# Kernel optimization log

Hardware: AMD Instinct MI355X
Metric: run time of the kernel (lower is better)

The kernel has to match this reference:

```python
import jax, jax.numpy as jnp
import numpy as np

B, NP, L, C, NA = 16, 512, 20, 3, 50
RATIO = 0.8
K = int(np.ceil(RATIO * NP))  # 410 nodes kept per graph
N = B * NP
E = 6 * N
NF, EF = 13, 4
EPS = 1e-5


def _graph_norm(x, w, b, ms):
    # PyG GraphNorm called WITHOUT batch in the source -> single global graph
    mean = x.mean(0)
    out = x - ms * mean
    var = (out * out).mean(0)
    return w * out / jnp.sqrt(var + EPS) + b


def _forward(x, pan_w, lin1_w, lin1_b, norm1_w, norm1_b, norm1_ms,
             pool_p, pool_beta, gat_wl, gat_bl, gat_wr, gat_br, gat_att, gat_bias,
             norm2_w, norm2_b, norm2_ms,
             val1_w, val1_b, val2_w, val2_b, val3_w, val3_b,
             adv1_w, adv1_b, adv2_w, adv2_b, adv3_w, adv3_b,
             edge_index, current_node_ids, action_mask):
    src, dst = edge_index[0], edge_index[1]
    # PANConv builds SparseTensor(row=edge_index[1], col=edge_index[0]) -> row = target
    A = jnp.zeros((B, NP, NP), x.dtype).at[dst // NP, dst % NP, src % NP].set(1.0)
    eyeB = jnp.broadcast_to(jnp.eye(NP, dtype=x.dtype), A.shape)

    # panentropy: M = sum_{i=0..L} w_i * A^i  (dense per graph)
    def step(carry, wi):
        tmp, acc = carry
        tmp = tmp @ A
        return (tmp, acc + wi * tmp), None
    (_, M), _ = jax.lax.scan(step, (eyeB, pan_w[0] * eyeB), pan_w[1:])
    deg = M.sum(-1)                                   # row sums
    dis = jnp.where(deg > 0, 1.0 / jnp.sqrt(deg), 0.0)
    Mn = dis[:, :, None] * M * dis[:, None, :]        # D^-1/2 M D^-1/2

    # conv1: propagate (Mn @ x) then Linear
    x3 = x.reshape(B, NP, NF)
    h = jnp.einsum('bij,bjf->bif', Mn, x3) @ lin1_w + lin1_b   # [B,NP,C]
    x1 = jax.nn.relu(_graph_norm(h.reshape(N, C), norm1_w, norm1_b, norm1_ms))  # [N,C]
    h = x1.reshape(B, NP, C)

    # PANPooling: score = tanh(b0 * <x,p> + b1 * colsum(Mn)); keep top K per graph
    score = jnp.tanh(pool_beta[0] * (h * pool_p).sum(-1) + pool_beta[1] * Mn.sum(-2))
    vals, idx = jax.lax.top_k(score, K)                        # [B,K]
    xp = jnp.take_along_axis(h, idx[:, :, None], axis=1) * vals[..., None]
    Mg = jax.vmap(lambda m, i: m[i][:, i])(Mn, idx)            # filtered adjacency [B,K,K]
    mask = (jnp.swapaxes(Mg, 1, 2) != 0) | jnp.eye(K, dtype=bool)  # mask[b,i,j]: edge j->i (+self loops)

    # GATv2Conv, heads=1, eval mode (no dropout), edge_attr not passed in source
    xl = xp @ gat_wl + gat_bl
    xr = xp @ gat_wr + gat_br
    e = jax.nn.leaky_relu(xr[:, :, None, :] + xl[:, None, :, :], 0.2)  # [B,i,j,C]
    logits = jnp.where(mask, jnp.einsum('bijc,c->bij', e, gat_att), -1e9)
    alpha = jax.nn.softmax(logits, axis=-1)
    g = jnp.einsum('bij,bjc->bic', alpha, xl) + gat_bias

    g = jax.nn.relu(_graph_norm(g.reshape(B * K, C), norm2_w, norm2_b, norm2_ms)).reshape(B, K, C)
    gp = g.sum(1)                                              # global_add_pool [B,C]

    # source uses POOLED bincount cumsum offsets to index the pre-pool arrays (faithful)
    gidx = current_node_ids + jnp.arange(B, dtype=current_node_ids.dtype) * K
    feat = jnp.concatenate([x[gidx], x1[gidx], gp], axis=1)    # [B,19]

    a = jax.nn.relu(feat @ adv1_w + adv1_b)
    a = jax.nn.relu(a @ adv2_w + adv2_b)
    a = a @ adv3_w + adv3_b
    v = jax.nn.relu(feat @ val1_w + val1_b)
    v = jax.nn.relu(v @ val2_w + val2_b)
    v = v @ val3_w + val3_b
    q = v + (a - a.mean(1, keepdims=True))
    return jnp.where(action_mask == 0, -1e8, q)


def setup_inputs() -> dict:
    key = jax.random.key(0)
    ks = list(jax.random.split(key, 40))
    nk = lambda: ks.pop()
    # within-graph random edges so the PyG-style batch structure is valid
    g = jax.random.randint(nk(), (E,), 0, B)
    u = jax.random.randint(nk(), (E,), 0, NP)
    v = jax.random.randint(nk(), (E,), 0, NP)
    edge_index = jnp.stack([g * NP + u, g * NP + v]).astype(jnp.int32)

    def lin(k, i, o):
        k1, k2 = jax.random.split(k)
        return (jax.random.normal(k1, (i, o), jnp.float32) / np.sqrt(i),
                jax.random.normal(k2, (o,), jnp.float32) * 0.01)

    lin1_w, lin1_b = lin(nk(), NF, C)
    gat_wl, gat_bl = lin(nk(), C, C)
    gat_wr, gat_br = lin(nk(), C, C)
    val1_w, val1_b = lin(nk(), 19, 10)
    val2_w, val2_b = lin(nk(), 10, 5)
    val3_w, val3_b = lin(nk(), 5, 1)
    adv1_w, adv1_b = lin(nk(), 19, 10)
    adv2_w, adv2_b = lin(nk(), 10, 5)
    adv3_w, adv3_b = lin(nk(), 5, NA)
    return dict(
        x=jax.random.normal(nk(), (N, NF), jnp.float32),
        edge_index=edge_index,
        edge_attr=jax.random.normal(nk(), (E, EF), jnp.float32),
        batch=jnp.arange(N, dtype=jnp.int32) // NP,
        current_node_ids=jax.random.randint(nk(), (B,), 0, NP),
        action_mask=jax.random.randint(nk(), (B, NA), 0, 2),
        pan_w=jax.random.uniform(nk(), (L + 1,), jnp.float32) * 0.5,
        lin1_w=lin1_w, lin1_b=lin1_b,
        norm1_w=jnp.ones(C), norm1_b=jnp.zeros(C), norm1_ms=jnp.ones(C),
        pool_p=jax.random.normal(nk(), (C,), jnp.float32),
        pool_beta=jnp.array([0.5, 0.5], jnp.float32),
        gat_wl=gat_wl, gat_bl=gat_bl, gat_wr=gat_wr, gat_br=gat_br,
        gat_att=jax.random.normal(nk(), (C,), jnp.float32),
        gat_bias=jax.random.normal(nk(), (C,), jnp.float32) * 0.01,
        norm2_w=jnp.ones(C), norm2_b=jnp.zeros(C), norm2_ms=jnp.ones(C),
        val1_w=val1_w, val1_b=val1_b, val2_w=val2_w, val2_b=val2_b,
        val3_w=val3_w, val3_b=val3_b,
        adv1_w=adv1_w, adv1_b=adv1_b, adv2_w=adv2_w, adv2_b=adv2_b,
        adv3_w=adv3_w, adv3_b=adv3_b,
    )


def reference(x, edge_index, edge_attr, batch, current_node_ids, action_mask,
              pan_w, lin1_w, lin1_b, norm1_w, norm1_b, norm1_ms,
              pool_p, pool_beta, gat_wl, gat_bl, gat_wr, gat_br, gat_att, gat_bias,
              norm2_w, norm2_b, norm2_ms,
              val1_w, val1_b, val2_w, val2_b, val3_w, val3_b,
              adv1_w, adv1_b, adv2_w, adv2_b, adv3_w, adv3_b):
    del edge_attr, batch  # received by the torch forward but never consumed
    return _forward(x, pan_w, lin1_w, lin1_b, norm1_w, norm1_b, norm1_ms,
                    pool_p, pool_beta, gat_wl, gat_bl, gat_wr, gat_br, gat_att, gat_bias,
                    norm2_w, norm2_b, norm2_ms,
                    val1_w, val1_b, val2_w, val2_b, val3_w, val3_b,
                    adv1_w, adv1_b, adv2_w, adv2_b, adv3_w, adv3_b,
                    edge_index, current_node_ids, action_mask)
```

## Files before the change

kernel.cpp:

```cpp
#include <hip/hip_runtime.h>
#include <stdint.h>
#include <math.h>

#define BB   16
#define NPn  512
#define LLp  20
#define NAa  50
#define KKk  410
#define NNt  (BB * NPn)
#define EEe  (6 * NNt)
#define NFf  13
#define KPAD 416
#define KP2  448
#define EPSf 1e-5f
#define QCLMP 1e6f
#define MAXD 28
#define PADR 512

__device__ __forceinline__ float r17_sane(float v) {
    if (!(v == v)) return 0.0f;
    return fminf(fmaxf(v, -1e15f), 1e15f);
}

__device__ __forceinline__ int r19_wmaxdeg(const int (&iF)[MAXD]) {
    int deg = 0;
#pragma unroll
    for (int j = 0; j < MAXD; ++j) deg += (iF[j] != PADR) ? 1 : 0;
#pragma unroll
    for (int off = 32; off; off >>= 1) {
        const int o = __shfl_xor(deg, off);
        deg = o > deg ? o : deg;
    }
    return deg;
}

__device__ __forceinline__ float r19_gsum(const float* __restrict__ rp,
                                          const int (&iF)[MAXD], int dm) {
    float s = 0.0f;
    s += rp[iF[0]]; s += rp[iF[1]]; s += rp[iF[2]]; s += rp[iF[3]];
    if (dm > 4) {
        s += rp[iF[4]]; s += rp[iF[5]]; s += rp[iF[6]]; s += rp[iF[7]];
        if (dm > 8) {
            s += rp[iF[8]]; s += rp[iF[9]]; s += rp[iF[10]]; s += rp[iF[11]];
            if (dm > 12) {
                s += rp[iF[12]]; s += rp[iF[13]]; s += rp[iF[14]]; s += rp[iF[15]];
                if (dm > 16) {
                    s += rp[iF[16]]; s += rp[iF[17]]; s += rp[iF[18]]; s += rp[iF[19]];
                    if (dm > 20) {
                        s += rp[iF[20]]; s += rp[iF[21]]; s += rp[iF[22]]; s += rp[iF[23]];
                        if (dm > 24) {
                            s += rp[iF[24]]; s += rp[iF[25]]; s += rp[iF[26]]; s += rp[iF[27]];
                        }
                    }
                }
            }
        }
    }
    return s;
}

__device__ __forceinline__ void r19_gor(const uint2* __restrict__ rp,
                                        const int (&iF)[MAXD], int dm, uint2& r) {
    {
        const uint2 v0 = rp[iF[0]], v1 = rp[iF[1]], v2 = rp[iF[2]], v3 = rp[iF[3]];
        r.x |= v0.x | v1.x | v2.x | v3.x;
        r.y |= v0.y | v1.y | v2.y | v3.y;
    }
    if (dm > 4) {
        const uint2 v0 = rp[iF[4]], v1 = rp[iF[5]], v2 = rp[iF[6]], v3 = rp[iF[7]];
        r.x |= v0.x | v1.x | v2.x | v3.x;
        r.y |= v0.y | v1.y | v2.y | v3.y;
        if (dm > 8) {
            const uint2 w0 = rp[iF[8]], w1 = rp[iF[9]], w2 = rp[iF[10]], w3 = rp[iF[11]];
            r.x |= w0.x | w1.x | w2.x | w3.x;
            r.y |= w0.y | w1.y | w2.y | w3.y;
            if (dm > 12) {
                const uint2 u0 = rp[iF[12]], u1 = rp[iF[13]], u2 = rp[iF[14]], u3 = rp[iF[15]];
                r.x |= u0.x | u1.x | u2.x | u3.x;
                r.y |= u0.y | u1.y | u2.y | u3.y;
                if (dm > 16) {
                    const uint2 a0 = rp[iF[16]], a1 = rp[iF[17]], a2 = rp[iF[18]], a3 = rp[iF[19]];
                    r.x |= a0.x | a1.x | a2.x | a3.x;
                    r.y |= a0.y | a1.y | a2.y | a3.y;
                    if (dm > 20) {
                        const uint2 b0 = rp[iF[20]], b1 = rp[iF[21]], b2 = rp[iF[22]], b3 = rp[iF[23]];
                        r.x |= b0.x | b1.x | b2.x | b3.x;
                        r.y |= b0.y | b1.y | b2.y | b3.y;
                        if (dm > 24) {
                            const uint2 c0 = rp[iF[24]], c1 = rp[iF[25]], c2 = rp[iF[26]], c3 = rp[iF[27]];
                            r.x |= c0.x | c1.x | c2.x | c3.x;
                            r.y |= c0.y | c1.y | c2.y | c3.y;
                        }
                    }
                }
            }
        }
    }
}

__global__ __launch_bounds__(256) void r17_scatter(
    const int* __restrict__ ei,
    uint32_t* __restrict__ fwdb, uint32_t* __restrict__ trsb)
{
    const int e = blockIdx.x * 256 + threadIdx.x;
    if (e < EEe) {
        const int src = ei[e], dst = ei[EEe + e];
        atomicOr(&fwdb[(size_t)dst * 16 + ((src & 511) >> 5)], 1u << (src & 31));
        atomicOr(&trsb[(size_t)src * 16 + ((dst & 511) >> 5)], 1u << (dst & 31));
    }
}

__global__ __launch_bounds__(512) void r23_extract(
    const uint32_t* __restrict__ fwdb, const uint32_t* __restrict__ trsb,
    const float* __restrict__ panw,
    unsigned short* __restrict__ csrF, unsigned short* __restrict__ csrT,
    float* __restrict__ d0g)
{
    __shared__ __align__(16) uint32_t S[7168 + 1047];
    const int blk = blockIdx.x, tid = threadIdx.x;

    if (blk < 32) {
        const int t = blk * 512 + tid;
        const int node = t & 8191;
        const uint32_t* bs = (t < 8192) ? (fwdb + (size_t)node * 16)
                                        : (trsb + (size_t)node * 16);
        unsigned short* cs = (t < 8192) ? csrF : csrT;
        int cnt = 0;
        for (int w = 0; w < 16; ++w) {
            uint32_t bits = bs[w];
            while (bits) {
                const int u = (w << 5) + __ffs(bits) - 1;
                bits &= bits - 1;
                if (cnt < MAXD) cs[(size_t)cnt * 8192 + node] = (unsigned short)u;
                ++cnt;
            }
        }
        for (int j = cnt; j < MAXD; ++j) cs[(size_t)j * 8192 + node] = PADR;
    } else {
        const int b = blk - 32;
        const int node = b * 512 + tid;
        unsigned short* Ctmp = (unsigned short*)S;
        float* pa  = (float*)(S + 7168);
        float* pb  = pa + 513;
        float* wsh = pb + 513;
        {
            const uint32_t* bs = fwdb + (size_t)node * 16;
            int cnt = 0;
            for (int w = 0; w < 16; ++w) {
                uint32_t bits = bs[w];
                while (bits) {
                    const int u = (w << 5) + __ffs(bits) - 1;
                    bits &= bits - 1;
                    if (cnt < MAXD) Ctmp[cnt * 512 + tid] = (unsigned short)u;
                    ++cnt;
                }
            }
            for (int j = cnt; j < MAXD; ++j) Ctmp[j * 512 + tid] = PADR;
        }
        int iF[MAXD];
#pragma unroll
        for (int j = 0; j < MAXD; ++j) iF[j] = (int)Ctmp[j * 512 + tid];
        const int dmF = r19_wmaxdeg(iF);

        if (tid < 21) wsh[tid] = panw[tid];
        pa[tid] = 1.0f;
        if (tid == 0) { pa[512] = 0.0f; pb[512] = 0.0f; }
        __syncthreads();
        float dacc = wsh[0];
        {
            float* rp = pa; float* rn = pb;
            for (int i = 1; i <= LLp; ++i) {
                const float s = r19_gsum(rp, iF, dmF);
                rn[tid] = s;
                dacc += wsh[i] * s;
                __syncthreads();
                float* tp = rp; rp = rn; rn = tp;
            }
        }
        d0g[node] = (dacc > 0.0f) ? 1.0f / sqrtf(dacc) : 0.0f;
    }
}

__global__ __launch_bounds__(512) void r23_mid(
    const float* __restrict__ x,
    const unsigned short* __restrict__ csrF,
    const unsigned short* __restrict__ csrT,
    const float* __restrict__ panw,
    const float* __restrict__ l1w, const float* __restrict__ l1b,
    const float* __restrict__ d0g,
    float* __restrict__ h_raw, float* __restrict__ colsum,
    uint32_t* __restrict__ Rb)
{
    __shared__ __align__(16) uint32_t sbuf[2052];
    const int b = blockIdx.x, y = blockIdx.y, t = threadIdx.x;
    const int node = b * 512 + t;

    if (y < 4) {
        const int c = y;
        float* pa  = (float*)sbuf;
        float* pb  = (float*)(sbuf + 513);
        float* wsh = (float*)(sbuf + 1026);
        if (t < 21) wsh[t] = panw[t];

        int idx[MAXD];
        if (c == 3) {
#pragma unroll
            for (int j = 0; j < MAXD; ++j) idx[j] = (int)csrT[(size_t)j * 8192 + node];
        } else {
#pragma unroll
            for (int j = 0; j < MAXD; ++j) idx[j] = (int)csrF[(size_t)j * 8192 + node];
        }
        const int dm2 = r19_wmaxdeg(idx);
        const float d0 = d0g[node];

        float seed;
        if (c < 3) {
            float xw = 0.0f;
            const float* xr = x + (size_t)node * NFf;
            for (int f = 0; f < NFf; ++f) xw += xr[f] * l1w[f * 3 + c];
            seed = d0 * xw;
        } else {
            seed = d0;
        }
        pa[t] = seed;
        if (t == 0) { pa[512] = 0.0f; pb[512] = 0.0f; }
        __syncthreads();
        float acc = wsh[0] * seed;
        {
            float* rp = pa; float* rn = pb;
            for (int i = 1; i <= LLp; ++i) {
                const float s = r19_gsum(rp, idx, dm2);
                rn[t] = s;
                acc += wsh[i] * s;
                __syncthreads();
                float* tp = rp; rp = rn; rn = tp;
            }
        }
        if (c < 3) h_raw[(size_t)node * 3 + c] = r17_sane(d0 * acc + l1b[c]);
        else       colsum[node] = r17_sane(d0 * acc);
    } else {
        int iF[MAXD];
#pragma unroll
        for (int j = 0; j < MAXD; ++j) iF[j] = (int)csrF[(size_t)j * 8192 + node];
        const int dmF = r19_wmaxdeg(iF);
        const int q = y - 4;
        uint2* R1 = (uint2*)sbuf;
        uint2* R2 = R1 + 513;
        uint2 seed;
        seed.x = ((t >> 5) == 2 * q)     ? (1u << (t & 31)) : 0u;
        seed.y = ((t >> 5) == 2 * q + 1) ? (1u << (t & 31)) : 0u;
        R1[t] = seed;
        if (t == 0) {
            uint2 z; z.x = 0u; z.y = 0u;
            R1[512] = z; R2[512] = z;
        }
        __syncthreads();
        uint2* Rp = R1; uint2* Rn = R2;
        for (int i = 0; i < LLp; ++i) {
            uint2 r = Rp[t];
            r19_gor(Rp, iF, dmF, r);
            Rn[t] = r;
            __syncthreads();
            uint2* tp = Rp; Rp = Rn; Rn = tp;
        }
        *(uint2*)(&Rb[(size_t)node * 16 + 2 * q]) = Rp[t];
    }
}

__global__ __launch_bounds__(512) void r19_pool(
    const float* __restrict__ h_raw,
    const float* __restrict__ colsum,
    const uint32_t* __restrict__ Rb,
    const float* n1w, const float* n1b, const float* n1ms,
    const float* poolp, const float* poolb,
    const float* gwl, const float* gbl,
    float* __restrict__ x1,
    float* __restrict__ xpg,
    float4* __restrict__ xlg,
    int*   __restrict__ kidxg,
    uint32_t* __restrict__ RTg)
{
    __shared__ __align__(16) uint32_t pg[2208];
    float* sc   = (float*)pg;
    float* mv   = (float*)(pg + 512);
    float* wred = (float*)(pg + 520);
    float* xpS  = (float*)(pg + 544);
    int*   kidx = (int*)(pg + 1792);
    const int b = blockIdx.x, t = threadIdx.x;
    const int lane = t & 63, wv = t >> 6;
    const float inv_n = 1.0f / (float)NNt;

    float hv0[16], hv1[16], hv2[16];
    float p0 = 0.0f, p1 = 0.0f, p2 = 0.0f;
#pragma unroll
    for (int k = 0; k < 16; ++k) {
        const float* hr = h_raw + (size_t)(k * 512 + t) * 3;
        hv0[k] = hr[0]; hv1[k] = hr[1]; hv2[k] = hr[2];
        p0 += hv0[k]; p1 += hv1[k]; p2 += hv2[k];
    }
#pragma unroll
    for (int off = 32; off; off >>= 1) {
        p0 += __shfl_xor(p0, off); p1 += __shfl_xor(p1, off); p2 += __shfl_xor(p2, off);
    }
    if (lane == 0) { wred[wv * 3 + 0] = p0; wred[wv * 3 + 1] = p1; wred[wv * 3 + 2] = p2; }
    __syncthreads();
    if (t < 3) {
        float s = 0.0f;
        for (int w = 0; w < 8; ++w) s += wred[w * 3 + t];
        mv[t] = s * inv_n;
    }
    __syncthreads();
    const float mm0 = n1ms[0] * mv[0], mm1 = n1ms[1] * mv[1], mm2 = n1ms[2] * mv[2];
    float q0 = 0.0f, q1 = 0.0f, q2 = 0.0f;
#pragma unroll
    for (int k = 0; k < 16; ++k) {
        const float d0 = hv0[k] - mm0, d1 = hv1[k] - mm1, d2 = hv2[k] - mm2;
        q0 += d0 * d0; q1 += d1 * d1; q2 += d2 * d2;
    }
#pragma unroll
    for (int off = 32; off; off >>= 1) {
        q0 += __shfl_xor(q0, off); q1 += __shfl_xor(q1, off); q2 += __shfl_xor(q2, off);
    }
    if (lane == 0) { wred[wv * 3 + 0] = q0; wred[wv * 3 + 1] = q1; wred[wv * 3 + 2] = q2; }
    __syncthreads();
    if (t < 3) {
        float s = 0.0f;
        for (int w = 0; w < 8; ++w) s += wred[w * 3 + t];
        mv[3 + t] = s * inv_n;
    }
    __syncthreads();

    const float mmv[3] = { mm0, mm1, mm2 };
    float xv[3];
#pragma unroll
    for (int c = 0; c < 3; ++c) {
        const float iv = 1.0f / sqrtf(fmaxf(mv[3 + c], 0.0f) + EPSf);
        const float o  = h_raw[(size_t)(b * NPn + t) * 3 + c] - mmv[c];
        const float tt = n1w[c] * o * iv + n1b[c];
        xv[c] = fmaxf(tt, 0.0f);
        x1[(size_t)(b * NPn + t) * 3 + c] = xv[c];
    }
    float s = poolb[0] * (xv[0] * poolp[0] + xv[1] * poolp[1] + xv[2] * poolp[2])
            + poolb[1] * colsum[b * NPn + t];
    s = tanhf(s);
    if (!(s == s)) s = 0.0f;
    sc[t] = s;
    __syncthreads();

    int cnt = 0;
    for (int u = 0; u < NPn; u += 4) {
        const float4 s4 = *(const float4*)(sc + u);
        cnt += ((s4.x > s) || (s4.x == s && (u + 0) < t)) ? 1 : 0;
        cnt += ((s4.y > s) || (s4.y == s && (u + 1) < t)) ? 1 : 0;
        cnt += ((s4.z > s) || (s4.z == s && (u + 2) < t)) ? 1 : 0;
        cnt += ((s4.w > s) || (s4.w == s && (u + 3) < t)) ? 1 : 0;
    }
    if (cnt < KKk) {
        const float xp0 = xv[0] * s, xp1 = xv[1] * s, xp2 = xv[2] * s;
        kidx[cnt] = t;
        xpS[cnt * 3 + 0] = xp0;
        xpS[cnt * 3 + 1] = xp1;
        xpS[cnt * 3 + 2] = xp2;
        kidxg[b * KPAD + cnt] = t;
        xpg[(size_t)(b * KPAD + cnt) * 3 + 0] = xp0;
        xpg[(size_t)(b * KPAD + cnt) * 3 + 1] = xp1;
        xpg[(size_t)(b * KPAD + cnt) * 3 + 2] = xp2;
    }
    __syncthreads();

    float Wl[9];
#pragma unroll
    for (int i2 = 0; i2 < 9; ++i2) Wl[i2] = gwl[i2];
    const float Bl0 = gbl[0], Bl1 = gbl[1], Bl2 = gbl[2];
    if (t < KP2) {
        float xl0, xl1, xl2;
        uint32_t* RT = RTg + (size_t)b * 16 * KP2 + t;
        if (t < KKk) {
            const float c0 = xpS[t * 3 + 0];
            const float c1 = xpS[t * 3 + 1];
            const float c2 = xpS[t * 3 + 2];
            xl0 = c0 * Wl[0] + c1 * Wl[3] + c2 * Wl[6] + Bl0;
            xl1 = c0 * Wl[1] + c1 * Wl[4] + c2 * Wl[7] + Bl1;
            xl2 = c0 * Wl[2] + c1 * Wl[5] + c2 * Wl[8] + Bl2;
            const uint4* rr = (const uint4*)(Rb + (size_t)(b * NPn + kidx[t]) * 16);
            const uint4 r0 = rr[0], r1 = rr[1], r2 = rr[2], r3 = rr[3];
            RT[ 0 * KP2] = r0.x; RT[ 1 * KP2] = r0.y; RT[ 2 * KP2] = r0.z; RT[ 3 * KP2] = r0.w;
            RT[ 4 * KP2] = r1.x; RT[ 5 * KP2] = r1.y; RT[ 6 * KP2] = r1.z; RT[ 7 * KP2] = r1.w;
            RT[ 8 * KP2] = r2.x; RT[ 9 * KP2] = r2.y; RT[10 * KP2] = r2.z; RT[11 * KP2] = r2.w;
            RT[12 * KP2] = r3.x; RT[13 * KP2] = r3.y; RT[14 * KP2] = r3.z; RT[15 * KP2] = r3.w;
        } else {
            xl0 = 0.0f; xl1 = 0.0f; xl2 = 0.0f;
#pragma unroll
            for (int w = 0; w < 16; ++w) RT[w * KP2] = 0u;
        }
        xlg[(size_t)(b * KP2 + t)] = make_float4(xl0, xl1, xl2, 0.0f);
    }
}

__global__ __launch_bounds__(512) void r19_gat(
    const float* __restrict__ xpg,
    const float4* __restrict__ xlg,
    const int* __restrict__ kidxg,
    const uint32_t* __restrict__ RTg,
    const float* __restrict__ gwr, const float* __restrict__ gbr,
    const float* __restrict__ gatt, const float* __restrict__ gbias,
    float* __restrict__ g_raw)
{
    const int b = blockIdx.x, y = blockIdx.y, t = threadIdx.x;
    const int lane = t & 63, wv = t >> 6;
    const int i = y * 8 + wv;
    if (i >= KKk) return;

    float Wr[9];
#pragma unroll
    for (int k = 0; k < 9; ++k) Wr[k] = gwr[k];
    const float Br0 = gbr[0], Br1 = gbr[1], Br2 = gbr[2];
    const float At0 = gatt[0], At1 = gatt[1], At2 = gatt[2];
    const float Gb0 = gbias[0], Gb1 = gbias[1], Gb2 = gbias[2];

    const int bi = kidxg[b * KPAD + i];
    const float c0 = xpg[(size_t)(b * KPAD + i) * 3 + 0];
    const float c1 = xpg[(size_t)(b * KPAD + i) * 3 + 1];
    const float c2 = xpg[(size_t)(b * KPAD + i) * 3 + 2];
    const float xr0 = c0 * Wr[0] + c1 * Wr[3] + c2 * Wr[6] + Br0;
    const float xr1 = c0 * Wr[1] + c1 * Wr[4] + c2 * Wr[7] + Br1;
    const float xr2 = c0 * Wr[2] + c1 * Wr[5] + c2 * Wr[8] + Br2;

    const uint32_t mbit = 1u << (bi & 31);
    const uint32_t* Rw = RTg + (size_t)(b * 16 + (bi >> 5)) * KP2;
    const float4* xlb = xlg + (size_t)b * KP2;

    float mx = -3e38f, lsum = 0.0f, b0 = 0.0f, b1 = 0.0f, b2 = 0.0f;
#pragma unroll
    for (int it = 0; it < 7; ++it) {
        const int j = lane + it * 64;
        const uint32_t rw = Rw[j];
        const float4 xlv = xlb[j];
        const float xl0 = xlv.x, xl1 = xlv.y, xl2 = xlv.z;
        const bool valid = (rw & mbit) || (j == i);
        float e0 = xr0 + xl0; e0 = e0 > 0.0f ? e0 : 0.2f * e0;
        float e1 = xr1 + xl1; e1 = e1 > 0.0f ? e1 : 0.2f * e1;
        float e2 = xr2 + xl2; e2 = e2 > 0.0f ? e2 : 0.2f * e2;
        const float sv = At0 * e0 + At1 * e1 + At2 * e2;
        if (valid) {
            if (sv > mx) {
                const float r = __expf(mx - sv);
                lsum *= r; b0 *= r; b1 *= r; b2 *= r;
                mx = sv;
            }
            const float pj = __expf(sv - mx);
            lsum += pj;
            b0 += pj * xl0; b1 += pj * xl1; b2 += pj * xl2;
        }
    }
#pragma unroll
    for (int off = 32; off; off >>= 1) {
        const float mo = __shfl_xor(mx, off);
        const float lo = __shfl_xor(lsum, off);
        const float d0 = __shfl_xor(b0, off);
        const float d1 = __shfl_xor(b1, off);
        const float d2 = __shfl_xor(b2, off);
        const float M  = fmaxf(mx, mo);
        const float ea = __expf(mx - M), eb = __expf(mo - M);
        lsum = lsum * ea + lo * eb;
        b0 = b0 * ea + d0 * eb;
        b1 = b1 * ea + d1 * eb;
        b2 = b2 * ea + d2 * eb;
        mx = M;
    }
    if (lane == 0) {
        const float rl = 1.0f / fmaxf(lsum, 1e-30f);
        g_raw[(size_t)(b * KPAD + i) * 3 + 0] = r17_sane(b0 * rl + Gb0);
        g_raw[(size_t)(b * KPAD + i) * 3 + 1] = r17_sane(b1 * rl + Gb1);
        g_raw[(size_t)(b * KPAD + i) * 3 + 2] = r17_sane(b2 * rl + Gb2);
    }
}

__global__ __launch_bounds__(512) void r17_head(
    const float* __restrict__ g_raw,
    const float* __restrict__ x1,
    const float* __restrict__ x,
    const int* __restrict__ cnid,
    const int* __restrict__ amask,
    const float* n2w, const float* n2b, const float* n2ms,
    const float* v1w, const float* v1b,
    const float* v2w, const float* v2b,
    const float* v3w, const float* v3b,
    const float* a1w, const float* a1b,
    const float* a2w, const float* a2b,
    const float* a3w, const float* a3b,
    float* __restrict__ out)
{
    __shared__ float wred[24];
    __shared__ float mv[6];
    __shared__ float gp[3];
    __shared__ float feat[19];
    __shared__ float h1a[10], h1v[10], h2a[5], h2v[5];
    __shared__ float a3[50];
    __shared__ float vout_s, amean_s;
    const int b = blockIdx.x, t = threadIdx.x;
    const int lane = t & 63, wv = t >> 6;
    const float denom = 1.0f / (float)(BB * KKk);

    float gv0[13], gv1[13], gv2[13];
    float p0 = 0.0f, p1 = 0.0f, p2 = 0.0f;
#pragma unroll
    for (int k = 0; k < 13; ++k) {
        const int r = k * 512 + t;
        float q0 = 0.0f, q1 = 0.0f, q2 = 0.0f;
        if (r < BB * KKk) {
            const int bq = r / KKk, iq = r - bq * KKk;
            const float* gr = g_raw + (size_t)(bq * KPAD + iq) * 3;
            q0 = gr[0]; q1 = gr[1]; q2 = gr[2];
        }
        gv0[k] = q0; gv1[k] = q1; gv2[k] = q2;
        p0 += q0; p1 += q1; p2 += q2;
    }
#pragma unroll
    for (int off = 32; off; off >>= 1) {
        p0 += __shfl_xor(p0, off); p1 += __shfl_xor(p1, off); p2 += __shfl_xor(p2, off);
    }
    if (lane == 0) { wred[wv * 3 + 0] = p0; wred[wv * 3 + 1] = p1; wred[wv * 3 + 2] = p2; }
    __syncthreads();
    if (t < 3) {
        float s = 0.0f;
        for (int w = 0; w < 8; ++w) s += wred[w * 3 + t];
        mv[t] = s * denom;
    }
    __syncthreads();
    const float mm0 = n2ms[0] * mv[0], mm1 = n2ms[1] * mv[1], mm2 = n2ms[2] * mv[2];
    float q0a = 0.0f, q1a = 0.0f, q2a = 0.0f;
#pragma unroll
    for (int k = 0; k < 13; ++k) {
        const int r = k * 512 + t;
        if (r < BB * KKk) {
            const float d0 = gv0[k] - mm0, d1 = gv1[k] - mm1, d2 = gv2[k] - mm2;
            q0a += d0 * d0; q1a += d1 * d1; q2a += d2 * d2;
        }
    }
#pragma unroll
    for (int off = 32; off; off >>= 1) {
        q0a += __shfl_xor(q0a, off); q1a += __shfl_xor(q1a, off); q2a += __shfl_xor(q2a, off);
    }
    if (lane == 0) { wred[wv * 3 + 0] = q0a; wred[wv * 3 + 1] = q1a; wred[wv * 3 + 2] = q2a; }
    __syncthreads();
    if (t < 3) {
        float s = 0.0f;
        for (int w = 0; w < 8; ++w) s += wred[w * 3 + t];
        mv[3 + t] = s * denom;
    }
    __syncthreads();

    const float mmv[3] = { mm0, mm1, mm2 };
    float s3[3] = { 0.0f, 0.0f, 0.0f };
    if (t < KKk) {
        const size_t r = (size_t)(b * KPAD + t) * 3;
#pragma unroll
        for (int c = 0; c < 3; ++c) {
            const float iv = 1.0f / sqrtf(fmaxf(mv[3 + c], 0.0f) + EPSf);
            s3[c] = fmaxf((g_raw[r + c] - mmv[c]) * iv * n2w[c] + n2b[c], 0.0f);
        }
    }
    float g0 = s3[0], g1 = s3[1], g2 = s3[2];
#pragma unroll
    for (int off = 32; off; off >>= 1) {
        g0 += __shfl_xor(g0, off); g1 += __shfl_xor(g1, off); g2 += __shfl_xor(g2, off);
    }
    if (lane == 0) { wred[wv * 3 + 0] = g0; wred[wv * 3 + 1] = g1; wred[wv * 3 + 2] = g2; }
    __syncthreads();
    if (t < 3) {
        float s = 0.0f;
        for (int w = 0; w < 8; ++w) s += wred[w * 3 + t];
        gp[t] = s;
    }
    __syncthreads();

    if (t < 19) {
        const int gidx = cnid[b] + b * KKk;
        float fv;
        if (t < 13)      fv = x[(size_t)gidx * NFf + t];
        else if (t < 16) fv = x1[(size_t)gidx * 3 + (t - 13)];
        else             fv = gp[t - 16];
        feat[t] = fv;
    }
    __syncthreads();

    if (t < 10) {
        float s = a1b[t];
        for (int f = 0; f < 19; ++f) s += feat[f] * a1w[f * 10 + t];
        h1a[t] = fmaxf(s, 0.0f);
    } else if (t >= 64 && t < 74) {
        const int j = t - 64;
        float s = v1b[j];
        for (int f = 0; f < 19; ++f) s += feat[f] * v1w[f * 10 + j];
        h1v[j] = fmaxf(s, 0.0f);
    }
    __syncthreads();
    if (t < 5) {
        float s = a2b[t];
        for (int k = 0; k < 10; ++k) s += h1a[k] * a2w[k * 5 + t];
        h2a[t] = fmaxf(s, 0.0f);
    } else if (t >= 64 && t < 69) {
        const int j = t - 64;
        float s = v2b[j];
        for (int k = 0; k < 10; ++k) s += h1v[k] * v2w[k * 5 + j];
        h2v[j] = fmaxf(s, 0.0f);
    }
    __syncthreads();
    if (t < 50) {
        float s = a3b[t];
        for (int k = 0; k < 5; ++k) s += h2a[k] * a3w[k * 50 + t];
        a3[t] = s;
    } else if (t == 64) {
        float s = v3b[0];
        for (int k = 0; k < 5; ++k) s += h2v[k] * v3w[k];
        vout_s = s;
    }
    __syncthreads();
    if (t == 0) {
        float s = 0.0f;
        for (int k = 0; k < 50; ++k) s += a3[k];
        amean_s = s * (1.0f / 50.0f);
    }
    __syncthreads();
    if (t < 50) {
        float q = vout_s + a3[t] - amean_s;
        if (!(q == q)) q = 0.0f;
        q = fminf(fmaxf(q, -QCLMP), QCLMP);
        out[b * NAa + t] = (amask[b * NAa + t] == 0) ? -1e8f : q;
    }
}

extern "C" void kernel_launch(void* const* d_in, const int* in_sizes, int n_in,
                              void* d_out, int out_size, void* d_ws, size_t ws_size,
                              hipStream_t stream) {
    (void)in_sizes; (void)n_in; (void)out_size;
    const float* x     = (const float*)d_in[0];
    const int* ei      = (const int*)d_in[1];
    const int* cnid    = (const int*)d_in[4];
    const int* amask   = (const int*)d_in[5];
    const float* panw  = (const float*)d_in[6];
    const float* l1w   = (const float*)d_in[7];
    const float* l1b   = (const float*)d_in[8];
    const float* n1w   = (const float*)d_in[9];
    const float* n1b   = (const float*)d_in[10];
    const float* n1ms  = (const float*)d_in[11];
    const float* poolp = (const float*)d_in[12];
    const float* poolb = (const float*)d_in[13];
    const float* gwl   = (const float*)d_in[14];
    const float* gbl   = (const float*)d_in[15];
    const float* gwr   = (const float*)d_in[16];
    const float* gbr   = (const float*)d_in[17];
    const float* gatt  = (const float*)d_in[18];
    const float* gbias = (const float*)d_in[19];
    const float* n2w   = (const float*)d_in[20];
    const float* n2b   = (const float*)d_in[21];
    const float* n2ms  = (const float*)d_in[22];
    const float* v1w   = (const float*)d_in[23];
    const float* v1b   = (const float*)d_in[24];
    const float* v2w   = (const float*)d_in[25];
    const float* v2b   = (const float*)d_in[26];
    const float* v3w   = (const float*)d_in[27];
    const float* v3b   = (const float*)d_in[28];
    const float* a1w   = (const float*)d_in[29];
    const float* a1b   = (const float*)d_in[30];
    const float* a2w   = (const float*)d_in[31];
    const float* a2b   = (const float*)d_in[32];
    const float* a3w   = (const float*)d_in[33];
    const float* a3b   = (const float*)d_in[34];
    float* out         = (float*)d_out;

    uint8_t* wsb = (uint8_t*)d_ws;
    uint32_t* fwdb = (uint32_t*)wsb;
    uint32_t* trsb = (uint32_t*)(wsb + 524288);
    uint32_t* Rb   = (uint32_t*)(wsb + 1048576);
    unsigned short* csrF = (unsigned short*)(wsb + 1572864);
    unsigned short* csrT = csrF + (size_t)MAXD * 8192;
    float* d0g    = (float*)(csrT + (size_t)MAXD * 8192);
    float* h_raw  = d0g + NNt;
    float* x1     = h_raw + (size_t)NNt * 3;
    float* colsum = x1 + (size_t)NNt * 3;
    float* g_raw  = colsum + NNt;
    float* xpg    = g_raw + (size_t)BB * KPAD * 3;
    float4* xlg   = (float4*)(xpg + (size_t)BB * KPAD * 3);
    int*   kidxg  = (int*)(xlg + (size_t)BB * KP2);
    uint32_t* RTg = (uint32_t*)(kidxg + (size_t)BB * KPAD);
    const size_t needed = (size_t)((uint8_t*)(RTg + (size_t)BB * 16 * KP2) - wsb);
    if (ws_size < needed) return;

    hipMemsetAsync(fwdb, 0, 1048576, stream);
    r17_scatter<<<dim3((EEe + 255) / 256), dim3(256), 0, stream>>>(ei, fwdb, trsb);
    r23_extract<<<dim3(48), dim3(512), 0, stream>>>(fwdb, trsb, panw,
                                                    csrF, csrT, d0g);
    r23_mid<<<dim3(16, 12), dim3(512), 0, stream>>>(x, csrF, csrT, panw, l1w, l1b,
                                                    d0g, h_raw, colsum, Rb);
    r19_pool<<<dim3(16), dim3(512), 0, stream>>>(h_raw, colsum, Rb,
                                                 n1w, n1b, n1ms, poolp, poolb,
                                                 gwl, gbl,
                                                 x1, xpg, xlg, kidxg, RTg);
    r19_gat<<<dim3(16, 52), dim3(512), 0, stream>>>(xpg, xlg, kidxg, RTg,
                                                    gwr, gbr, gatt, gbias, g_raw);
    r17_head<<<dim3(16), dim3(512), 0, stream>>>(g_raw, x1, x, cnid, amask,
                                                 n2w, n2b, n2ms, v1w, v1b, v2w, v2b, v3w, v3b,
                                                 a1w, a1b, a2w, a2b, a3w, a3b, out);
}
```

Measured before the change: 202.3 us.

## Move reachability bitset propagation into extract kernel with early convergence exit

The boolean reachability propagation (8 blocks per graph) moves from the mid kernel into the extract kernel. It builds its neighbour list directly from the forward bitset, so it no longer waits for the CSR build and can overlap with the degree computation. A shared flag per iteration records whether any bit changed, and the loop exits once the set stops growing. The mid kernel now launches only the four float propagation blocks per graph. Whether the early exit helps depends on graph diameter, and the extra block-wide flag check adds a small cost to each iteration.

```diff
diff --git a/kernel.cpp b/kernel.cpp
--- a/kernel.cpp
+++ b/kernel.cpp
@@ -98,6 +98,22 @@
     }
 }
 
+__device__ __forceinline__ void r24_bsextract(
+    const uint32_t* __restrict__ bs, unsigned short* __restrict__ Ctmp, int tid)
+{
+    int cnt = 0;
+    for (int w = 0; w < 16; ++w) {
+        uint32_t bits = bs[w];
+        while (bits) {
+            const int u = (w << 5) + __ffs(bits) - 1;
+            bits &= bits - 1;
+            if (cnt < MAXD) Ctmp[cnt * 512 + tid] = (unsigned short)u;
+            ++cnt;
+        }
+    }
+    for (int j = cnt; j < MAXD; ++j) Ctmp[j * 512 + tid] = PADR;
+}
+
 __global__ __launch_bounds__(256) void r17_scatter(
     const int* __restrict__ ei,
     uint32_t* __restrict__ fwdb, uint32_t* __restrict__ trsb)
@@ -110,13 +126,13 @@
     }
 }
 
-__global__ __launch_bounds__(512) void r23_extract(
+__global__ __launch_bounds__(512) void r24_extract(
     const uint32_t* __restrict__ fwdb, const uint32_t* __restrict__ trsb,
     const float* __restrict__ panw,
     unsigned short* __restrict__ csrF, unsigned short* __restrict__ csrT,
-    float* __restrict__ d0g)
+    float* __restrict__ d0g, uint32_t* __restrict__ Rb)
 {
-    __shared__ __align__(16) uint32_t S[7168 + 1047];
+    __shared__ __align__(16) uint32_t S[9240];
     const int blk = blockIdx.x, tid = threadIdx.x;
 
     if (blk < 32) {
@@ -136,27 +152,14 @@
             }
         }
         for (int j = cnt; j < MAXD; ++j) cs[(size_t)j * 8192 + node] = PADR;
-    } else {
+    } else if (blk < 48) {
         const int b = blk - 32;
         const int node = b * 512 + tid;
         unsigned short* Ctmp = (unsigned short*)S;
         float* pa  = (float*)(S + 7168);
         float* pb  = pa + 513;
         float* wsh = pb + 513;
-        {
-            const uint32_t* bs = fwdb + (size_t)node * 16;
-            int cnt = 0;
-            for (int w = 0; w < 16; ++w) {
-                uint32_t bits = bs[w];
-                while (bits) {
-                    const int u = (w << 5) + __ffs(bits) - 1;
-                    bits &= bits - 1;
-                    if (cnt < MAXD) Ctmp[cnt * 512 + tid] = (unsigned short)u;
-                    ++cnt;
-                }
-            }
-            for (int j = cnt; j < MAXD; ++j) Ctmp[j * 512 + tid] = PADR;
-        }
+        r24_bsextract(fwdb + (size_t)node * 16, Ctmp, tid);
         int iF[MAXD];
 #pragma unroll
         for (int j = 0; j < MAXD; ++j) iF[j] = (int)Ctmp[j * 512 + tid];
@@ -178,93 +181,99 @@
             }
         }
         d0g[node] = (dacc > 0.0f) ? 1.0f / sqrtf(dacc) : 0.0f;
-    }
-}
-
-__global__ __launch_bounds__(512) void r23_mid(
+    } else {
+        const int rix = blk - 48;
+        const int b = rix >> 3, q = rix & 7;
+        const int node = b * 512 + tid;
+        unsigned short* Ctmp = (unsigned short*)S;
+        uint2* R1 = (uint2*)(S + 7168);
+        uint2* R2 = R1 + 513;
+        uint32_t* flags = (uint32_t*)(R2 + 513);
+        r24_bsextract(fwdb + (size_t)node * 16, Ctmp, tid);
+        int iF[MAXD];
+#pragma unroll
+        for (int j = 0; j < MAXD; ++j) iF[j] = (int)Ctmp[j * 512 + tid];
+        const int dmF = r19_wmaxdeg(iF);
+
+        uint2 seed;
+        seed.x = ((tid >> 5) == 2 * q)     ? (1u << (tid & 31)) : 0u;
+        seed.y = ((tid >> 5) == 2 * q + 1) ? (1u << (tid & 31)) : 0u;
+        R1[tid] = seed;
+        if (tid == 0) {
+            uint2 z; z.x = 0u; z.y = 0u;
+            R1[512] = z; R2[512] = z;
+        }
+        if (tid < LLp) flags[tid] = 0u;
+        __syncthreads();
+        uint2* Rp = R1; uint2* Rn = R2;
+        for (int i = 0; i < LLp; ++i) {
+            uint2 r = Rp[tid];
+            const uint2 old = r;
+            r19_gor(Rp, iF, dmF, r);
+            Rn[tid] = r;
+            if ((r.x != old.x) | (r.y != old.y)) flags[i] = 1u;
+            __syncthreads();
+            uint2* tp = Rp; Rp = Rn; Rn = tp;
+            if (flags[i] == 0u) break;
+        }
+        *(uint2*)(&Rb[(size_t)node * 16 + 2 * q]) = Rp[tid];
+    }
+}
+
+__global__ __launch_bounds__(512) void r24_mid(
     const float* __restrict__ x,
     const unsigned short* __restrict__ csrF,
     const unsigned short* __restrict__ csrT,
     const float* __restrict__ panw,
     const float* __restrict__ l1w, const float* __restrict__ l1b,
     const float* __restrict__ d0g,
-    float* __restrict__ h_raw, float* __restrict__ colsum,
-    uint32_t* __restrict__ Rb)
+    float* __restrict__ h_raw, float* __restrict__ colsum)
 {
-    __shared__ __align__(16) uint32_t sbuf[2052];
-    const int b = blockIdx.x, y = blockIdx.y, t = threadIdx.x;
+    __shared__ __align__(16) uint32_t sbuf[1047];
+    const int b = blockIdx.x, c = blockIdx.y, t = threadIdx.x;
     const int node = b * 512 + t;
 
-    if (y < 4) {
-        const int c = y;
-        float* pa  = (float*)sbuf;
-        float* pb  = (float*)(sbuf + 513);
-        float* wsh = (float*)(sbuf + 1026);
-        if (t < 21) wsh[t] = panw[t];
-
-        int idx[MAXD];
-        if (c == 3) {
-#pragma unroll
-            for (int j = 0; j < MAXD; ++j) idx[j] = (int)csrT[(size_t)j * 8192 + node];
-        } else {
-#pragma unroll
-            for (int j = 0; j < MAXD; ++j) idx[j] = (int)csrF[(size_t)j * 8192 + node];
-        }
-        const int dm2 = r19_wmaxdeg(idx);
-        const float d0 = d0g[node];
-
-        float seed;
-        if (c < 3) {
-            float xw = 0.0f;
-            const float* xr = x + (size_t)node * NFf;
-            for (int f = 0; f < NFf; ++f) xw += xr[f] * l1w[f * 3 + c];
-            seed = d0 * xw;
-        } else {
-            seed = d0;
-        }
-        pa[t] = seed;
-        if (t == 0) { pa[512] = 0.0f; pb[512] = 0.0f; }
-        __syncthreads();
-        float acc = wsh[0] * seed;
-        {
-            float* rp = pa; float* rn = pb;
-            for (int i = 1; i <= LLp; ++i) {
-                const float s = r19_gsum(rp, idx, dm2);
-                rn[t] = s;
-                acc += wsh[i] * s;
-                __syncthreads();
-                float* tp = rp; rp = rn; rn = tp;
-            }
-        }
-        if (c < 3) h_raw[(size_t)node * 3 + c] = r17_sane(d0 * acc + l1b[c]);
-        else       colsum[node] = r17_sane(d0 * acc);
+    float* pa  = (float*)sbuf;
+    float* pb  = (float*)(sbuf + 513);
+    float* wsh = (float*)(sbuf + 1026);
+    if (t < 21) wsh[t] = panw[t];
+
+    int idx[MAXD];
+    if (c == 3) {
+#pragma unroll
+        for (int j = 0; j < MAXD; ++j) idx[j] = (int)csrT[(size_t)j * 8192 + node];
     } else {
-        int iF[MAXD];
-#pragma unroll
-        for (int j = 0; j < MAXD; ++j) iF[j] = (int)csrF[(size_t)j * 8192 + node];
-        const int dmF = r19_wmaxdeg(iF);
-        const int q = y - 4;
-        uint2* R1 = (uint2*)sbuf;
-        uint2* R2 = R1 + 513;
-        uint2 seed;
-        seed.x = ((t >> 5) == 2 * q)     ? (1u << (t & 31)) : 0u;
-        seed.y = ((t >> 5) == 2 * q + 1) ? (1u << (t & 31)) : 0u;
-        R1[t] = seed;
-        if (t == 0) {
-            uint2 z; z.x = 0u; z.y = 0u;
-            R1[512] = z; R2[512] = z;
-        }
-        __syncthreads();
-        uint2* Rp = R1; uint2* Rn = R2;
-        for (int i = 0; i < LLp; ++i) {
-            uint2 r = Rp[t];
-            r19_gor(Rp, iF, dmF, r);
-            Rn[t] = r;
+#pragma unroll
+        for (int j = 0; j < MAXD; ++j) idx[j] = (int)csrF[(size_t)j * 8192 + node];
+    }
+    const int dm2 = r19_wmaxdeg(idx);
+    const float d0 = d0g[node];
+
+    float seed;
+    if (c < 3) {
+        float xw = 0.0f;
+        const float* xr = x + (size_t)node * NFf;
+        for (int f = 0; f < NFf; ++f) xw += xr[f] * l1w[f * 3 + c];
+        seed = d0 * xw;
+    } else {
+        seed = d0;
+    }
+    pa[t] = seed;
+    if (t == 0) { pa[512] = 0.0f; pb[512] = 0.0f; }
+    __syncthreads();
+    float acc = wsh[0] * seed;
+    {
+        float* rp = pa; float* rn = pb;
+        for (int i = 1; i <= LLp; ++i) {
+            const float s = r19_gsum(rp, idx, dm2);
+            rn[t] = s;
+            acc += wsh[i] * s;
             __syncthreads();
-            uint2* tp = Rp; Rp = Rn; Rn = tp;
-        }
-        *(uint2*)(&Rb[(size_t)node * 16 + 2 * q]) = Rp[t];
-    }
+            float* tp = rp; rp = rn; rn = tp;
+        }
+    }
+    if (c < 3) h_raw[(size_t)node * 3 + c] = r17_sane(d0 * acc + l1b[c]);
+    else       colsum[node] = r17_sane(d0 * acc);
 }
 
 __global__ __launch_bounds__(512) void r19_pool(
@@ -690,10 +699,10 @@
 
     hipMemsetAsync(fwdb, 0, 1048576, stream);
     r17_scatter<<<dim3((EEe + 255) / 256), dim3(256), 0, stream>>>(ei, fwdb, trsb);
-    r23_extract<<<dim3(48), dim3(512), 0, stream>>>(fwdb, trsb, panw,
-                                                    csrF, csrT, d0g);
-    r23_mid<<<dim3(16, 12), dim3(512), 0, stream>>>(x, csrF, csrT, panw, l1w, l1b,
-                                                    d0g, h_raw, colsum, Rb);
+    r24_extract<<<dim3(176), dim3(512), 0, stream>>>(fwdb, trsb, panw,
+                                                     csrF, csrT, d0g, Rb);
+    r24_mid<<<dim3(16, 4), dim3(512), 0, stream>>>(x, csrF, csrT, panw, l1w, l1b,
+                                                   d0g, h_raw, colsum);
     r19_pool<<<dim3(16), dim3(512), 0, stream>>>(h_raw, colsum, Rb,
                                                  n1w, n1b, n1ms, poolp, poolb,
                                                  gwl, gbl,
```

Result: no change. 201.5 us (-0.4%).
